# Kernel optimization log

Measured on AMD Instinct MI355X. Metric: run time of the kernel, lower is better.

## Reference

```python
import jax, jax.numpy as jnp
import numpy as np

B, S, D, H = 2, 2048, 1024, 16
DK = D // H


def setup_inputs() -> dict:
    key = jax.random.key(0)
    ks = jax.random.split(key, 11)
    s = 1.0 / np.sqrt(D)
    inp = {
        "q": jax.random.normal(ks[0], (B, S, D), jnp.float32),
        "k": jax.random.normal(ks[1], (B, S, D), jnp.float32),
        "v": jax.random.normal(ks[2], (B, S, D), jnp.float32),
        # causal (lower-triangular) decoder mask, broadcast over batch & heads
        "mask": jnp.tril(jnp.ones((S, S), jnp.int32))[None, None, :, :],
        "Wq": jax.random.normal(ks[3], (D, D), jnp.float32) * s,
        "bq": jax.random.normal(ks[4], (D,), jnp.float32) * s,
        "Wk": jax.random.normal(ks[5], (D, D), jnp.float32) * s,
        "bk": jax.random.normal(ks[6], (D,), jnp.float32) * s,
        "Wv": jax.random.normal(ks[7], (D, D), jnp.float32) * s,
        "bv": jax.random.normal(ks[8], (D,), jnp.float32) * s,
        "Wo": jax.random.normal(ks[9], (D, D), jnp.float32) * s,
        "bo": jax.random.normal(ks[10], (D,), jnp.float32) * s,
    }
    return inp


def reference(q, k, v, mask, Wq, bq, Wk, bk, Wv, bv, Wo, bo):
    # projections (nn.Linear: x @ W.T + b)
    def proj(x, W, b):
        return (x @ W.T + b).reshape(B, S, H, DK).transpose(0, 2, 1, 3)  # [B,H,S,DK]

    Q = proj(q, Wq, bq)
    K = proj(k, Wk, bk)
    V = proj(v, Wv, bv)

    scores = jnp.einsum("bhsd,bhtd->bhst", Q, K) / jnp.sqrt(jnp.float32(DK))
    scores = jnp.where(mask == 0, jnp.float32(-1e9), scores)
    attn = jax.nn.softmax(scores, axis=-1)  # dropout=0.0 -> identity
    ctx = jnp.einsum("bhst,bhtd->bhsd", attn, V)
    ctx = ctx.transpose(0, 2, 1, 3).reshape(B, S, D)
    return ctx @ Wo.T + bo
```

## Files before the change

### kernel.cpp

```cpp
#include <hip/hip_runtime.h>

typedef __bf16 bf16;
typedef __bf16 bf16x8 __attribute__((ext_vector_type(8)));
typedef float floatx4 __attribute__((ext_vector_type(4)));

#define NB 2
#define NS 2048
#define ND 1024
#define NH 16
#define NDK 64
#define NM (NB * NS)

__device__ __forceinline__ void async_cp16(const void* g, void* l) {
  __builtin_amdgcn_global_load_lds(
      (const __attribute__((address_space(1))) void*)g,
      (__attribute__((address_space(3))) void*)l, 16, 0, 0);
}

__device__ __forceinline__ bf16x8 cvt8(const float* p) {
  float4 lo = *(const float4*)p, hi = *(const float4*)(p + 4);
  bf16x8 o;
  o[0] = (bf16)lo.x; o[1] = (bf16)lo.y; o[2] = (bf16)lo.z; o[3] = (bf16)lo.w;
  o[4] = (bf16)hi.x; o[5] = (bf16)hi.y; o[6] = (bf16)hi.z; o[7] = (bf16)hi.w;
  return o;
}

__device__ __forceinline__ void wg_barrier_lds() {
  __asm__ __volatile__("s_waitcnt lgkmcnt(0)" ::: "memory");
  __builtin_amdgcn_s_barrier();
}

struct CvtArgs {
  const float* src[8];
  bf16* dst[8];
  int nblk[8];
  int nseg;
};

__global__ __launch_bounds__(256) void cvt_kernel(CvtArgs a) {
  int b = blockIdx.x, seg = 0;
  while (seg < a.nseg - 1 && b >= a.nblk[seg]) { b -= a.nblk[seg]; ++seg; }
  const size_t idx = ((size_t)b * 256 + threadIdx.x) * 8;
  *(bf16x8*)(a.dst[seg] + idx) = cvt8(a.src[seg] + idx);
}

template <int TM, typename TA, typename TC>
__global__ __launch_bounds__(256) void gemm_dma(
    const TA* __restrict__ A0, const TA* __restrict__ A1, const TA* __restrict__ A2,
    const bf16* __restrict__ W0, const bf16* __restrict__ W1, const bf16* __restrict__ W2,
    const float* __restrict__ bias0, const float* __restrict__ bias1, const float* __restrict__ bias2,
    TC* __restrict__ C0, TC* __restrict__ C1, TC* __restrict__ C2)
{
  const int z = blockIdx.z;
  const TA* A = (z == 0) ? A0 : (z == 1) ? A1 : A2;
  const bf16* W = (z == 0) ? W0 : (z == 1) ? W1 : W2;
  const float* bias = (z == 0) ? bias0 : (z == 1) ? bias1 : bias2;
  TC* C = (z == 0) ? C0 : (z == 1) ? C1 : C2;

  __shared__ bf16 At[TM * 32];
  __shared__ bf16 Bt[128 * 32];

  const int tid = threadIdx.x;
  const int wave = tid >> 6, lane = tid & 63;
  const int q4 = lane >> 4, l15 = lane & 15;
  const int m0 = blockIdx.y * TM, n0 = blockIdx.x * 128;
  constexpr int WM = TM / 2;
  constexpr int MI = WM / 16;
  const int wm = (wave >> 1) * WM, wn = (wave & 1) * 64;

  floatx4 acc[MI][4] = {};

  const bf16* Wg = W + (size_t)(n0 + (lane >> 2)) * ND + (lane & 3) * 8;
  const bf16* Ag = nullptr;
  const float* Af = nullptr;
  const int srow = tid >> 2, sk = (tid & 3) * 8;
  if constexpr (sizeof(TA) == 2)
    Ag = (const bf16*)A + (size_t)(m0 + (lane >> 2)) * ND + (lane & 3) * 8;
  else
    Af = (const float*)A + (size_t)(m0 + srow) * ND + sk;

  for (int k0 = 0; k0 < ND; k0 += 32) {
    bf16x8 a0, a1;
    if constexpr (sizeof(TA) == 4) {
      a0 = cvt8(Af + k0);
      if constexpr (TM == 128) a1 = cvt8(Af + (size_t)64 * ND + k0);
    }
    __syncthreads();
#pragma unroll
    for (int c2 = 0; c2 < 2; ++c2) {
      const int c = wave * 2 + c2;
      async_cp16(Wg + (size_t)c * 16 * ND + k0, &Bt[c * 16 * 32]);
    }
    if constexpr (sizeof(TA) == 2) {
#pragma unroll
      for (int c2 = 0; c2 < TM / 64; ++c2) {
        const int c = wave * (TM / 64) + c2;
        async_cp16(Ag + (size_t)c * 16 * ND + k0, &At[c * 16 * 32]);
      }
    } else {
      *(bf16x8*)&At[srow * 32 + sk] = a0;
      if constexpr (TM == 128) *(bf16x8*)&At[(srow + 64) * 32 + sk] = a1;
    }
    __syncthreads();

    bf16x8 af[MI], bfr[4];
#pragma unroll
    for (int i = 0; i < MI; ++i)
      af[i] = *(const bf16x8*)&At[(wm + i * 16 + l15) * 32 + q4 * 8];
#pragma unroll
    for (int j = 0; j < 4; ++j)
      bfr[j] = *(const bf16x8*)&Bt[(wn + j * 16 + l15) * 32 + q4 * 8];
#pragma unroll
    for (int i = 0; i < MI; ++i)
#pragma unroll
      for (int j = 0; j < 4; ++j)
        acc[i][j] = __builtin_amdgcn_mfma_f32_16x16x32_bf16(af[i], bfr[j], acc[i][j], 0, 0, 0);
  }

#pragma unroll
  for (int j = 0; j < 4; ++j) {
    const int col = n0 + wn + j * 16 + l15;
    const float bv = bias[col];
#pragma unroll
    for (int i = 0; i < MI; ++i) {
      const int rowb = m0 + wm + i * 16 + q4 * 4;
#pragma unroll
      for (int r = 0; r < 4; ++r)
        C[(size_t)(rowb + r) * ND + col] = (TC)(acc[i][j][r] + bv);
    }
  }
}

#define NEGBIG (-1e30f)
#define LDV 72

__global__ __launch_bounds__(256) void attn_kernel(
    const bf16* __restrict__ Q, const bf16* __restrict__ K,
    const bf16* __restrict__ V, bf16* __restrict__ O)
{
  __shared__ bf16 vt[2][64 * LDV];
  __shared__ bf16 pbuf[4][16 * LDV];

  const int bx = blockIdx.x;
  const int h = blockIdx.y, b = blockIdx.z;
  const int tid = threadIdx.x, wave = tid >> 6, lane = tid & 63;
  const int q4 = lane >> 4, l15 = lane & 15;
  const int sl = lane;
  const int dbase = wave * 8;

  const bf16* kp = K + ((size_t)(b * NS) + l15) * ND + h * NDK + q4 * 8;
  const bf16* vp = V + ((size_t)(b * NS) + sl) * ND + h * NDK + dbase;

  bf16x8 qf[2];
  floatx4 oacc[4];
  float psum[4];
  bf16x8 kA[8], vA[2], kB[8], vB[2];

  auto ldK = [&](int j, bf16x8 (&kk)[8]) {
    const bf16* p = kp + (size_t)j * (64 * ND);
#pragma unroll
    for (int nf = 0; nf < 4; ++nf)
#pragma unroll
      for (int t = 0; t < 2; ++t)
        kk[nf * 2 + t] = *(const bf16x8*)(p + (size_t)nf * 16 * ND + t * 32);
  };
  auto ldV = [&](int j, bf16x8 (&vv)[2]) {
    const bf16* p = vp + (size_t)j * (64 * ND);
    vv[0] = *(const bf16x8*)(p);
    vv[1] = *(const bf16x8*)(p + 32);
  };

  auto body = [&](int j, int iq, bf16x8 (&kc)[8], bf16x8 (&vc)[2],
                  bf16x8 (&kn)[8], bf16x8 (&vn)[2]) {
    const int cur = j & 1;
#pragma unroll
    for (int it = 0; it < 2; ++it)
#pragma unroll
      for (int e = 0; e < 8; ++e)
        vt[cur][(dbase + it * 32 + e) * LDV + sl] = vc[it][e];

    if (j < iq) ldV(j + 1, vn);

    floatx4 sf[4];
    __builtin_amdgcn_s_setprio(1);
#pragma unroll
    for (int nf = 0; nf < 4; ++nf) {
      floatx4 s = {0.f, 0.f, 0.f, 0.f};
      s = __builtin_amdgcn_mfma_f32_16x16x32_bf16(qf[0], kc[nf * 2 + 0], s, 0, 0, 0);
      s = __builtin_amdgcn_mfma_f32_16x16x32_bf16(qf[1], kc[nf * 2 + 1], s, 0, 0, 0);
      sf[nf] = s;
    }
    __builtin_amdgcn_s_setprio(0);

    if (j < iq) ldK(j + 1, kn);

    wg_barrier_lds();

    if (j == iq) {
#pragma unroll
      for (int nf = 0; nf < 4; ++nf) {
        const int kc2 = nf * 16 + l15;
#pragma unroll
        for (int r = 0; r < 4; ++r)
          if (kc2 > wave * 16 + q4 * 4 + r) sf[nf][r] = NEGBIG;
      }
    }

#pragma unroll
    for (int nf = 0; nf < 4; ++nf)
#pragma unroll
      for (int r = 0; r < 4; ++r) {
        const float pv = exp2f(sf[nf][r]);
        psum[r] += pv;
        pbuf[wave][(q4 * 4 + r) * LDV + nf * 16 + l15] = (bf16)pv;
      }
    __asm__ __volatile__("s_waitcnt lgkmcnt(0)" ::: "memory");

    __builtin_amdgcn_s_setprio(1);
#pragma unroll
    for (int nf = 0; nf < 4; ++nf)
#pragma unroll
      for (int t = 0; t < 2; ++t) {
        bf16x8 pa = *(const bf16x8*)&pbuf[wave][l15 * LDV + t * 32 + q4 * 8];
        bf16x8 vb = *(const bf16x8*)&vt[cur][(nf * 16 + l15) * LDV + t * 32 + q4 * 8];
        oacc[nf] = __builtin_amdgcn_mfma_f32_16x16x32_bf16(pa, vb, oacc[nf], 0, 0, 0);
      }
    __builtin_amdgcn_s_setprio(0);
  };

  for (int ph = 0; ph < 2; ++ph) {
    const int iq = ph ? (31 - bx) : bx;
    __syncthreads();

    const size_t qrow0 = (size_t)(b * NS + iq * 64 + wave * 16 + l15);
#pragma unroll
    for (int t = 0; t < 2; ++t) {
      bf16x8 tmp = *(const bf16x8*)(Q + qrow0 * ND + h * NDK + t * 32 + q4 * 8);
#pragma unroll
      for (int e = 0; e < 8; ++e) qf[t][e] = (bf16)((float)tmp[e] * 0.180336880f);
    }

#pragma unroll
    for (int nf = 0; nf < 4; ++nf) oacc[nf] = floatx4{0.f, 0.f, 0.f, 0.f};
#pragma unroll
    for (int r = 0; r < 4; ++r) psum[r] = 0.f;

    ldK(0, kA); ldV(0, vA);
    for (int j = 0; j <= iq; ++j) {
      if ((j & 1) == 0) body(j, iq, kA, vA, kB, vB);
      else              body(j, iq, kB, vB, kA, vA);
    }

#pragma unroll
    for (int r = 0; r < 4; ++r)
#pragma unroll
      for (int off = 1; off < 16; off <<= 1) psum[r] += __shfl_xor(psum[r], off, 16);

#pragma unroll
    for (int nf = 0; nf < 4; ++nf)
#pragma unroll
      for (int r = 0; r < 4; ++r) {
        const int qrow = iq * 64 + wave * 16 + q4 * 4 + r;
        O[(size_t)(b * NS + qrow) * ND + h * NDK + nf * 16 + l15] =
            (bf16)(oacc[nf][r] / psum[r]);
      }
  }
}

extern "C" void kernel_launch(void* const* d_in, const int* in_sizes, int n_in,
                              void* d_out, int out_size, void* d_ws, size_t ws_size,
                              hipStream_t stream) {
  const float* q  = (const float*)d_in[0];
  const float* k  = (const float*)d_in[1];
  const float* v  = (const float*)d_in[2];
  const float* Wq = (const float*)d_in[4];
  const float* bq = (const float*)d_in[5];
  const float* Wk = (const float*)d_in[6];
  const float* bk = (const float*)d_in[7];
  const float* Wv = (const float*)d_in[8];
  const float* bv = (const float*)d_in[9];
  const float* Wo = (const float*)d_in[10];
  const float* bo = (const float*)d_in[11];
  float* out = (float*)d_out;
  char* w = (char*)d_ws;

  const dim3 attn_grid(NS / 128, NH, NB);

  if (ws_size >= (size_t)56 << 20) {
    bf16* xq = (bf16*)(w);
    bf16* xk = (bf16*)(w + ((size_t)8 << 20));
    bf16* xv = (bf16*)(w + ((size_t)16 << 20));
    bf16* wq = (bf16*)(w + ((size_t)24 << 20));
    bf16* wk = (bf16*)(w + ((size_t)26 << 20));
    bf16* wv = (bf16*)(w + ((size_t)28 << 20));
    bf16* wo = (bf16*)(w + ((size_t)30 << 20));
    bf16* Qb = (bf16*)(w + ((size_t)32 << 20));
    bf16* Kb = (bf16*)(w + ((size_t)40 << 20));
    bf16* Vb = (bf16*)(w + ((size_t)48 << 20));
    bf16* Ob = xq;

    CvtArgs ca{};
    const int b4 = (int)((size_t)NM * ND / 2048);
    const int b1 = (int)((size_t)ND * ND / 2048);
    ca.src[0] = q;  ca.dst[0] = xq; ca.nblk[0] = b4;
    ca.src[1] = k;  ca.dst[1] = xk; ca.nblk[1] = b4;
    ca.src[2] = v;  ca.dst[2] = xv; ca.nblk[2] = b4;
    ca.src[3] = Wq; ca.dst[3] = wq; ca.nblk[3] = b1;
    ca.src[4] = Wk; ca.dst[4] = wk; ca.nblk[4] = b1;
    ca.src[5] = Wv; ca.dst[5] = wv; ca.nblk[5] = b1;
    ca.src[6] = Wo; ca.dst[6] = wo; ca.nblk[6] = b1;
    ca.nseg = 7;
    cvt_kernel<<<3 * b4 + 4 * b1, 256, 0, stream>>>(ca);

    gemm_dma<128, bf16, bf16><<<dim3(8, 32, 3), 256, 0, stream>>>(
        xq, xk, xv, wq, wk, wv, bq, bk, bv, Qb, Kb, Vb);
    attn_kernel<<<attn_grid, 256, 0, stream>>>(Qb, Kb, Vb, Ob);
    gemm_dma<64, bf16, float><<<dim3(8, 64, 1), 256, 0, stream>>>(
        Ob, Ob, Ob, wo, wo, wo, bo, bo, bo, out, out, out);
  } else if (ws_size >= (size_t)40 << 20) {
    bf16* wq = (bf16*)(w);
    bf16* wk = (bf16*)(w + ((size_t)2 << 20));
    bf16* wv = (bf16*)(w + ((size_t)4 << 20));
    bf16* wo = (bf16*)(w + ((size_t)6 << 20));
    bf16* Qb = (bf16*)(w + ((size_t)8 << 20));
    bf16* Kb = (bf16*)(w + ((size_t)16 << 20));
    bf16* Vb = (bf16*)(w + ((size_t)24 << 20));
    bf16* Ob = (bf16*)(w + ((size_t)32 << 20));

    CvtArgs ca{};
    const int b1 = (int)((size_t)ND * ND / 2048);
    ca.src[0] = Wq; ca.dst[0] = wq; ca.nblk[0] = b1;
    ca.src[1] = Wk; ca.dst[1] = wk; ca.nblk[1] = b1;
    ca.src[2] = Wv; ca.dst[2] = wv; ca.nblk[2] = b1;
    ca.src[3] = Wo; ca.dst[3] = wo; ca.nblk[3] = b1;
    ca.nseg = 4;
    cvt_kernel<<<4 * b1, 256, 0, stream>>>(ca);

    gemm_dma<128, float, bf16><<<dim3(8, 32, 3), 256, 0, stream>>>(
        q, k, v, wq, wk, wv, bq, bk, bv, Qb, Kb, Vb);
    attn_kernel<<<attn_grid, 256, 0, stream>>>(Qb, Kb, Vb, Ob);
    gemm_dma<64, bf16, float><<<dim3(8, 64, 1), 256, 0, stream>>>(
        Ob, Ob, Ob, wo, wo, wo, bo, bo, bo, out, out, out);
  }
}
```

Measured before the change: 272.5 us.

## Widen GEMM K-tile to 64 with XOR-swizzled LDS and split attention blocks

The GEMM now stages 64-wide K slices per iteration into larger LDS tiles with an XOR swizzle on column offsets, halving the barrier count per K and aiming to reduce LDS bank conflicts. The attention kernel drops the paired-phase scheme (each block handling tiles bx and 31-bx) and instead launches one block per query tile, heaviest tiles first. Occupancy hints are added via launch_bounds minimum-blocks arguments. The trade-offs are more LDS per GEMM block, possible register pressure from the occupancy hints, and per-block load imbalance in attention that now relies on the hardware scheduler.

```diff
diff --git a/kernel.cpp b/kernel.cpp
--- a/kernel.cpp
+++ b/kernel.cpp
@@ -45,7 +45,7 @@
 }
 
 template <int TM, typename TA, typename TC>
-__global__ __launch_bounds__(256) void gemm_dma(
+__global__ __launch_bounds__(256, 3) void gemm_dma(
     const TA* __restrict__ A0, const TA* __restrict__ A1, const TA* __restrict__ A2,
     const bf16* __restrict__ W0, const bf16* __restrict__ W1, const bf16* __restrict__ W2,
     const float* __restrict__ bias0, const float* __restrict__ bias1, const float* __restrict__ bias2,
@@ -57,8 +57,8 @@
   const float* bias = (z == 0) ? bias0 : (z == 1) ? bias1 : bias2;
   TC* C = (z == 0) ? C0 : (z == 1) ? C1 : C2;
 
-  __shared__ bf16 At[TM * 32];
-  __shared__ bf16 Bt[128 * 32];
+  __shared__ bf16 At[TM * 64];
+  __shared__ bf16 Bt[128 * 64];
 
   const int tid = threadIdx.x;
   const int wave = tid >> 6, lane = tid & 63;
@@ -70,51 +70,61 @@
 
   floatx4 acc[MI][4] = {};
 
-  const bf16* Wg = W + (size_t)(n0 + (lane >> 2)) * ND + (lane & 3) * 8;
+  const int srow8 = lane >> 3;
+  const int scol = ((lane & 7) ^ srow8) * 8;
+  const bf16* Wg = W + (size_t)(n0 + srow8) * ND + scol;
   const bf16* Ag = nullptr;
   const float* Af = nullptr;
-  const int srow = tid >> 2, sk = (tid & 3) * 8;
+  const int frow = tid >> 3, fk = (tid & 7) * 8;
+  const int fkswz = fk ^ ((frow & 7) * 8);
   if constexpr (sizeof(TA) == 2)
-    Ag = (const bf16*)A + (size_t)(m0 + (lane >> 2)) * ND + (lane & 3) * 8;
+    Ag = (const bf16*)A + (size_t)(m0 + srow8) * ND + scol;
   else
-    Af = (const float*)A + (size_t)(m0 + srow) * ND + sk;
-
-  for (int k0 = 0; k0 < ND; k0 += 32) {
-    bf16x8 a0, a1;
+    Af = (const float*)A + (size_t)(m0 + frow) * ND + fk;
+
+  for (int k0 = 0; k0 < ND; k0 += 64) {
+    bf16x8 a[TM / 32];
     if constexpr (sizeof(TA) == 4) {
-      a0 = cvt8(Af + k0);
-      if constexpr (TM == 128) a1 = cvt8(Af + (size_t)64 * ND + k0);
+#pragma unroll
+      for (int r = 0; r < TM / 32; ++r)
+        a[r] = cvt8(Af + (size_t)r * 32 * ND + k0);
     }
     __syncthreads();
 #pragma unroll
-    for (int c2 = 0; c2 < 2; ++c2) {
-      const int c = wave * 2 + c2;
-      async_cp16(Wg + (size_t)c * 16 * ND + k0, &Bt[c * 16 * 32]);
+    for (int c2 = 0; c2 < 4; ++c2) {
+      const int c = wave * 4 + c2;
+      async_cp16(Wg + (size_t)c * 8 * ND + k0, &Bt[c * 8 * 64]);
     }
     if constexpr (sizeof(TA) == 2) {
 #pragma unroll
-      for (int c2 = 0; c2 < TM / 64; ++c2) {
-        const int c = wave * (TM / 64) + c2;
-        async_cp16(Ag + (size_t)c * 16 * ND + k0, &At[c * 16 * 32]);
+      for (int c2 = 0; c2 < TM / 32; ++c2) {
+        const int c = wave * (TM / 32) + c2;
+        async_cp16(Ag + (size_t)c * 8 * ND + k0, &At[c * 8 * 64]);
       }
     } else {
-      *(bf16x8*)&At[srow * 32 + sk] = a0;
-      if constexpr (TM == 128) *(bf16x8*)&At[(srow + 64) * 32 + sk] = a1;
+#pragma unroll
+      for (int r = 0; r < TM / 32; ++r)
+        *(bf16x8*)&At[(frow + r * 32) * 64 + fkswz] = a[r];
     }
     __syncthreads();
 
-    bf16x8 af[MI], bfr[4];
-#pragma unroll
-    for (int i = 0; i < MI; ++i)
-      af[i] = *(const bf16x8*)&At[(wm + i * 16 + l15) * 32 + q4 * 8];
-#pragma unroll
-    for (int j = 0; j < 4; ++j)
-      bfr[j] = *(const bf16x8*)&Bt[(wn + j * 16 + l15) * 32 + q4 * 8];
-#pragma unroll
-    for (int i = 0; i < MI; ++i)
+#pragma unroll
+    for (int t = 0; t < 2; ++t) {
+      const int kb = t * 32 + q4 * 8;
+      const int swz = (l15 & 7) * 8;
+      bf16x8 af[MI], bfr[4];
+#pragma unroll
+      for (int i = 0; i < MI; ++i)
+        af[i] = *(const bf16x8*)&At[(wm + i * 16 + l15) * 64 + (kb ^ swz)];
 #pragma unroll
       for (int j = 0; j < 4; ++j)
-        acc[i][j] = __builtin_amdgcn_mfma_f32_16x16x32_bf16(af[i], bfr[j], acc[i][j], 0, 0, 0);
+        bfr[j] = *(const bf16x8*)&Bt[(wn + j * 16 + l15) * 64 + (kb ^ swz)];
+#pragma unroll
+      for (int i = 0; i < MI; ++i)
+#pragma unroll
+        for (int j = 0; j < 4; ++j)
+          acc[i][j] = __builtin_amdgcn_mfma_f32_16x16x32_bf16(af[i], bfr[j], acc[i][j], 0, 0, 0);
+    }
   }
 
 #pragma unroll
@@ -134,14 +144,14 @@
 #define NEGBIG (-1e30f)
 #define LDV 72
 
-__global__ __launch_bounds__(256) void attn_kernel(
+__global__ __launch_bounds__(256, 4) void attn_kernel(
     const bf16* __restrict__ Q, const bf16* __restrict__ K,
     const bf16* __restrict__ V, bf16* __restrict__ O)
 {
   __shared__ bf16 vt[2][64 * LDV];
   __shared__ bf16 pbuf[4][16 * LDV];
 
-  const int bx = blockIdx.x;
+  const int iq = 31 - blockIdx.x;
   const int h = blockIdx.y, b = blockIdx.z;
   const int tid = threadIdx.x, wave = tid >> 6, lane = tid & 63;
   const int q4 = lane >> 4, l15 = lane & 15;
@@ -170,7 +180,7 @@
     vv[1] = *(const bf16x8*)(p + 32);
   };
 
-  auto body = [&](int j, int iq, bf16x8 (&kc)[8], bf16x8 (&vc)[2],
+  auto body = [&](int j, bf16x8 (&kc)[8], bf16x8 (&vc)[2],
                   bf16x8 (&kn)[8], bf16x8 (&vn)[2]) {
     const int cur = j & 1;
 #pragma unroll
@@ -228,43 +238,38 @@
     __builtin_amdgcn_s_setprio(0);
   };
 
-  for (int ph = 0; ph < 2; ++ph) {
-    const int iq = ph ? (31 - bx) : bx;
-    __syncthreads();
-
-    const size_t qrow0 = (size_t)(b * NS + iq * 64 + wave * 16 + l15);
-#pragma unroll
-    for (int t = 0; t < 2; ++t) {
-      bf16x8 tmp = *(const bf16x8*)(Q + qrow0 * ND + h * NDK + t * 32 + q4 * 8);
-#pragma unroll
-      for (int e = 0; e < 8; ++e) qf[t][e] = (bf16)((float)tmp[e] * 0.180336880f);
-    }
-
-#pragma unroll
-    for (int nf = 0; nf < 4; ++nf) oacc[nf] = floatx4{0.f, 0.f, 0.f, 0.f};
-#pragma unroll
-    for (int r = 0; r < 4; ++r) psum[r] = 0.f;
-
-    ldK(0, kA); ldV(0, vA);
-    for (int j = 0; j <= iq; ++j) {
-      if ((j & 1) == 0) body(j, iq, kA, vA, kB, vB);
-      else              body(j, iq, kB, vB, kA, vA);
-    }
-
-#pragma unroll
-    for (int r = 0; r < 4; ++r)
-#pragma unroll
-      for (int off = 1; off < 16; off <<= 1) psum[r] += __shfl_xor(psum[r], off, 16);
-
-#pragma unroll
-    for (int nf = 0; nf < 4; ++nf)
-#pragma unroll
-      for (int r = 0; r < 4; ++r) {
-        const int qrow = iq * 64 + wave * 16 + q4 * 4 + r;
-        O[(size_t)(b * NS + qrow) * ND + h * NDK + nf * 16 + l15] =
-            (bf16)(oacc[nf][r] / psum[r]);
-      }
-  }
+  const size_t qrow0 = (size_t)(b * NS + iq * 64 + wave * 16 + l15);
+#pragma unroll
+  for (int t = 0; t < 2; ++t) {
+    bf16x8 tmp = *(const bf16x8*)(Q + qrow0 * ND + h * NDK + t * 32 + q4 * 8);
+#pragma unroll
+    for (int e = 0; e < 8; ++e) qf[t][e] = (bf16)((float)tmp[e] * 0.180336880f);
+  }
+
+#pragma unroll
+  for (int nf = 0; nf < 4; ++nf) oacc[nf] = floatx4{0.f, 0.f, 0.f, 0.f};
+#pragma unroll
+  for (int r = 0; r < 4; ++r) psum[r] = 0.f;
+
+  ldK(0, kA); ldV(0, vA);
+  for (int j = 0; j <= iq; ++j) {
+    if ((j & 1) == 0) body(j, kA, vA, kB, vB);
+    else              body(j, kB, vB, kA, vA);
+  }
+
+#pragma unroll
+  for (int r = 0; r < 4; ++r)
+#pragma unroll
+    for (int off = 1; off < 16; off <<= 1) psum[r] += __shfl_xor(psum[r], off, 16);
+
+#pragma unroll
+  for (int nf = 0; nf < 4; ++nf)
+#pragma unroll
+    for (int r = 0; r < 4; ++r) {
+      const int qrow = iq * 64 + wave * 16 + q4 * 4 + r;
+      O[(size_t)(b * NS + qrow) * ND + h * NDK + nf * 16 + l15] =
+          (bf16)(oacc[nf][r] / psum[r]);
+    }
 }
 
 extern "C" void kernel_launch(void* const* d_in, const int* in_sizes, int n_in,
@@ -284,7 +289,7 @@
   float* out = (float*)d_out;
   char* w = (char*)d_ws;
 
-  const dim3 attn_grid(NS / 128, NH, NB);
+  const dim3 attn_grid(32, NH, NB);
 
   if (ws_size >= (size_t)56 << 20) {
     bf16* xq = (bf16*)(w);
```

Result: slower. 528.3 us (+93.8%).
